# Optimization experiments

Hardware: AMD Instinct MI355X
Metric: run time of the kernel (lower is better)

## Reference

```python
import jax, jax.numpy as jnp
import numpy as np

N_NODES = 100000
N_EDGES = 600000
HIDDEN = 128
BN_EPS = 1e-5


def setup_inputs() -> dict:
    key = jax.random.key(0)
    k_x, k_e, k_w, k_b, k_g = jax.random.split(key, 5)
    x = jax.random.normal(k_x, (N_NODES, HIDDEN), dtype=jnp.float32)
    edge_index = jax.random.randint(k_e, (2, N_EDGES), 0, N_NODES, dtype=jnp.int64)
    # GCNConv linear weight (no bias on the linear; bias added post-aggregation)
    scale = 1.0 / np.sqrt(HIDDEN)
    W = jax.random.uniform(k_w, (HIDDEN, HIDDEN), jnp.float32, -scale, scale)
    b = jax.random.uniform(k_b, (HIDDEN,), jnp.float32, -scale, scale)
    gamma = jnp.ones((HIDDEN,), jnp.float32)   # BatchNorm weight
    beta = jnp.zeros((HIDDEN,), jnp.float32)   # BatchNorm bias
    return {"x": x, "edge_index": edge_index, "W": W, "b": b, "gamma": gamma, "beta": beta}


def reference(x, edge_index, W, b, gamma, beta):
    N = x.shape[0]
    # ReLU then GCNConv linear transform: [N, D]
    h = jnp.matmul(jax.nn.relu(x), W)
    # Add self-loops (PyG GCNConv default)
    loops = jnp.arange(N, dtype=edge_index.dtype)
    row = jnp.concatenate([edge_index[0], loops])  # source nodes
    col = jnp.concatenate([edge_index[1], loops])  # target nodes
    # Symmetric normalization deg^{-1/2} with unit edge weights
    ones = jnp.ones(row.shape[0], dtype=h.dtype)
    deg = jax.ops.segment_sum(ones, col, num_segments=N)
    dinv = jnp.where(deg > 0, jax.lax.rsqrt(deg), 0.0)
    norm = dinv[row] * dinv[col]  # [E+N]
    # Gather -> scale -> scatter-add aggregation, then conv bias
    agg = jax.ops.segment_sum(norm[:, None] * h[row], col, num_segments=N)
    out = agg + b
    # BatchNorm1d (training mode: batch stats, biased variance)
    mean = jnp.mean(out, axis=0)
    var = jnp.var(out, axis=0)
    return gamma * (out - mean) * jax.lax.rsqrt(var + BN_EPS) + beta
```

## Files before the change

### kernel.cpp

```cpp
#include <hip/hip_runtime.h>

#define D 128
#define CAP 32
#define BN_EPS 1e-5f

typedef float floatx4 __attribute__((ext_vector_type(4)));
typedef __bf16 bf16x8 __attribute__((ext_vector_type(8)));

__device__ inline unsigned short f2bf(float f) {
    unsigned u; __builtin_memcpy(&u, &f, 4);
    unsigned r = (u + 0x7FFFu + ((u >> 16) & 1u)) >> 16;
    return (unsigned short)r;
}
__device__ inline float bflo(unsigned v) { unsigned x = v << 16; float f; __builtin_memcpy(&f, &x, 4); return f; }
__device__ inline float bfhi(unsigned v) { unsigned x = v & 0xFFFF0000u; float f; __builtin_memcpy(&f, &x, 4); return f; }

__global__ void setup_k(const unsigned* __restrict__ e, int* __restrict__ flag,
                        int* __restrict__ cursor, float* __restrict__ sums,
                        float* __restrict__ sumsq, const float* __restrict__ W,
                        unsigned short* __restrict__ Wt, int n_nodes) {
    int i = blockIdx.x * blockDim.x + threadIdx.x;
    if (i < n_nodes) cursor[i] = 0;
    if (i < D) { sums[i] = 0.f; sumsq[i] = 0.f; }
    if (i < D * D) {
        int n = i >> 7, k = i & 127;
        Wt[n * D + k] = f2bf(W[k * D + n]);
    }
    if (i == 0) {
        unsigned acc = 0;
        for (int k = 0; k < 64; ++k) acc |= e[2 * k + 1];
        *flag = (acc == 0u) ? 1 : 0;
    }
}

__global__ __launch_bounds__(256, 2) void gemm_k(const float* __restrict__ x,
                                                 const unsigned short* __restrict__ Wt,
                                                 unsigned short* __restrict__ h,
                                                 int n_mtiles) {
    int lane = threadIdx.x & 63;
    int wave = blockIdx.x * 4 + (threadIdx.x >> 6);
    int nw = gridDim.x * 4;
    int l15 = lane & 15;
    int quad = lane >> 4;

    bf16x8 Bf[4][8];
    for (int ks = 0; ks < 4; ++ks)
        for (int j = 0; j < 8; ++j)
            Bf[ks][j] = *(const bf16x8*)(Wt + (size_t)(j * 16 + l15) * D + ks * 32 + quad * 8);

    for (int mt = wave; mt < n_mtiles; mt += nw) {
        const float* xrow = x + (size_t)(mt * 16 + l15) * D + quad * 8;
        bf16x8 Af[4];
        for (int ks = 0; ks < 4; ++ks) {
            float4 a0 = *(const float4*)(xrow + ks * 32);
            float4 a1 = *(const float4*)(xrow + ks * 32 + 4);
            float av[8] = {a0.x, a0.y, a0.z, a0.w, a1.x, a1.y, a1.z, a1.w};
            union { unsigned short u[8]; bf16x8 v; } tmp;
            for (int jj = 0; jj < 8; ++jj) tmp.u[jj] = f2bf(fmaxf(av[jj], 0.0f));
            Af[ks] = tmp.v;
        }
        floatx4 acc[8];
        for (int j = 0; j < 8; ++j) acc[j] = (floatx4){0.f, 0.f, 0.f, 0.f};
        for (int ks = 0; ks < 4; ++ks)
            for (int j = 0; j < 8; ++j)
                acc[j] = __builtin_amdgcn_mfma_f32_16x16x32_bf16(Af[ks], Bf[ks][j], acc[j], 0, 0, 0);
        for (int j = 0; j < 8; ++j)
            for (int reg = 0; reg < 4; ++reg) {
                int rr = mt * 16 + quad * 4 + reg;
                int cc = j * 16 + l15;
                h[(size_t)rr * D + cc] = f2bf(acc[j][reg]);
            }
    }
}

__global__ __launch_bounds__(256) void bucket_k(const void* __restrict__ ep, const int* __restrict__ flag,
                                                int* __restrict__ cursor, int* __restrict__ bucket,
                                                int n_edges) {
    int e = blockIdx.x * blockDim.x + threadIdx.x;
    if (e >= n_edges) return;
    int r, c;
    if (*flag) {
        const long long* p = (const long long*)ep;
        r = (int)p[e]; c = (int)p[e + n_edges];
    } else {
        const int* p = (const int*)ep;
        r = p[e]; c = p[e + n_edges];
    }
    int pos = atomicAdd(&cursor[c], 1);
    if (pos < CAP) bucket[(size_t)c * CAP + pos] = r;
}

__global__ void dinv_k(const int* __restrict__ cursor, float* __restrict__ dinv, int n_nodes) {
    int i = blockIdx.x * blockDim.x + threadIdx.x;
    if (i < n_nodes) dinv[i] = rsqrtf(1.0f + (float)cursor[i]);
}

#define PREPD(s, rr) { int r_ = ((s) < degc) ? (rr) : node;              \
                       w##s = ((s) < degc) ? dinv[r_] : 0.0f;            \
                       hv##s = hp[(unsigned)r_ * 64u + lane]; }
#define ACC(s) { ax += w##s * bflo(hv##s); ay += w##s * bfhi(hv##s); }

__global__ __launch_bounds__(256) void agg_k(const unsigned short* __restrict__ h,
                                             const int* __restrict__ bucket,
                                             const int* __restrict__ cursor,
                                             const float* __restrict__ dinv,
                                             unsigned* __restrict__ aggb,
                                             int n_nodes) {
    int lane = threadIdx.x & 63;
    int node = blockIdx.x * 4 + (threadIdx.x >> 6);
    if (node >= n_nodes) return;
    const unsigned* hp = (const unsigned*)h;

    int deg = cursor[node];
    int degc = deg < CAP ? deg : CAP;
    float dc = dinv[node];

    unsigned v = hp[(unsigned)node * 64u + lane];
    float ax = dc * bflo(v), ay = dc * bfhi(v);
    const int* bk = bucket + (size_t)node * CAP;

    float w0=0,w1=0,w2=0,w3=0,w4=0,w5=0,w6=0,w7=0;
    unsigned hv0=0,hv1=0,hv2=0,hv3=0,hv4=0,hv5=0,hv6=0,hv7=0;

    if (degc > 0) { int4 b = *(const int4*)(bk);     PREPD(0,b.x) PREPD(1,b.y) PREPD(2,b.z) PREPD(3,b.w) }
    if (degc > 4) { int4 b = *(const int4*)(bk + 4); PREPD(4,b.x) PREPD(5,b.y) PREPD(6,b.z) PREPD(7,b.w) }

    if (degc <= 8) {
        ACC(0) ACC(1) ACC(2) ACC(3) ACC(4) ACC(5) ACC(6) ACC(7)
    } else {
        float w8=0,w9=0,w10=0,w11=0,w12=0,w13=0,w14=0,w15=0;
        unsigned hv8=0,hv9=0,hv10=0,hv11=0,hv12=0,hv13=0,hv14=0,hv15=0;
        { int4 b = *(const int4*)(bk + 8); PREPD(8,b.x) PREPD(9,b.y) PREPD(10,b.z) PREPD(11,b.w) }
        if (degc > 12) { int4 b = *(const int4*)(bk + 12); PREPD(12,b.x) PREPD(13,b.y) PREPD(14,b.z) PREPD(15,b.w) }
        ACC(0)  ACC(1)  ACC(2)  ACC(3)  ACC(4)  ACC(5)  ACC(6)  ACC(7)
        ACC(8)  ACC(9)  ACC(10) ACC(11) ACC(12) ACC(13) ACC(14) ACC(15)
        for (int e = 16; e < degc; ++e) {
            int r = bk[e];
            float dr = dinv[r];
            unsigned hh = hp[(unsigned)r * 64u + lane];
            ax += dr * bflo(hh); ay += dr * bfhi(hh);
        }
    }

    float ox = dc * ax, oy = dc * ay;
    aggb[(unsigned)node * 64u + lane] = ((unsigned)f2bf(oy) << 16) | (unsigned)f2bf(ox);
}

__global__ __launch_bounds__(256) void stats_k(const unsigned* __restrict__ aggb,
                                               float* __restrict__ sums, float* __restrict__ sumsq,
                                               int n_nodes) {
    __shared__ float red[256];
    int lane = threadIdx.x & 63;
    int wib = threadIdx.x >> 6;
    int wave = blockIdx.x * 4 + wib;
    int nw = gridDim.x * 4;
    float s0 = 0.f, s1 = 0.f, q0 = 0.f, q1 = 0.f;
    int n = wave;
    for (; n + 3 * nw < n_nodes; n += 4 * nw) {
        unsigned p0 = aggb[(size_t)n * 64 + lane];
        unsigned p1 = aggb[(size_t)(n + nw) * 64 + lane];
        unsigned p2 = aggb[(size_t)(n + 2 * nw) * 64 + lane];
        unsigned p3 = aggb[(size_t)(n + 3 * nw) * 64 + lane];
        float a0 = bflo(p0), b0 = bfhi(p0), a1 = bflo(p1), b1 = bfhi(p1);
        float a2 = bflo(p2), b2 = bfhi(p2), a3 = bflo(p3), b3 = bfhi(p3);
        s0 += a0 + a1 + a2 + a3;
        s1 += b0 + b1 + b2 + b3;
        q0 += a0 * a0 + a1 * a1 + a2 * a2 + a3 * a3;
        q1 += b0 * b0 + b1 * b1 + b2 * b2 + b3 * b3;
    }
    for (; n < n_nodes; n += nw) {
        unsigned p = aggb[(size_t)n * 64 + lane];
        float vx = bflo(p), vy = bfhi(p);
        s0 += vx; s1 += vy; q0 += vx * vx; q1 += vy * vy;
    }
    red[threadIdx.x] = s0; __syncthreads();
    if (wib == 0) atomicAdd(&sums[2 * lane], red[lane] + red[64 + lane] + red[128 + lane] + red[192 + lane]);
    __syncthreads();
    red[threadIdx.x] = s1; __syncthreads();
    if (wib == 0) atomicAdd(&sums[2 * lane + 1], red[lane] + red[64 + lane] + red[128 + lane] + red[192 + lane]);
    __syncthreads();
    red[threadIdx.x] = q0; __syncthreads();
    if (wib == 0) atomicAdd(&sumsq[2 * lane], red[lane] + red[64 + lane] + red[128 + lane] + red[192 + lane]);
    __syncthreads();
    red[threadIdx.x] = q1; __syncthreads();
    if (wib == 0) atomicAdd(&sumsq[2 * lane + 1], red[lane] + red[64 + lane] + red[128 + lane] + red[192 + lane]);
}

__global__ __launch_bounds__(256) void final_k(const unsigned* __restrict__ aggb,
                                               const float* __restrict__ sums, const float* __restrict__ sumsq,
                                               const float* __restrict__ gamma, const float* __restrict__ beta,
                                               float* __restrict__ out, int total4, float inv_n) {
    int i = blockIdx.x * blockDim.x + threadIdx.x;
    if (i >= total4) return;
    int idx = i * 4;
    int f = idx & (D - 1);
    float4 sm = *(const float4*)(sums + f);
    float4 sq = *(const float4*)(sumsq + f);
    float4 g  = *(const float4*)(gamma + f);
    float4 bt = *(const float4*)(beta + f);
    uint2 p = *(const uint2*)(aggb + i * 2);

    float m0 = sm.x * inv_n, m1 = sm.y * inv_n, m2 = sm.z * inv_n, m3 = sm.w * inv_n;
    float sc0 = g.x * rsqrtf(sq.x * inv_n - m0 * m0 + BN_EPS);
    float sc1 = g.y * rsqrtf(sq.y * inv_n - m1 * m1 + BN_EPS);
    float sc2 = g.z * rsqrtf(sq.z * inv_n - m2 * m2 + BN_EPS);
    float sc3 = g.w * rsqrtf(sq.w * inv_n - m3 * m3 + BN_EPS);
    float4 o;
    o.x = fmaf(bflo(p.x), sc0, bt.x - m0 * sc0);
    o.y = fmaf(bfhi(p.x), sc1, bt.y - m1 * sc1);
    o.z = fmaf(bflo(p.y), sc2, bt.z - m2 * sc2);
    o.w = fmaf(bfhi(p.y), sc3, bt.w - m3 * sc3);
    *(float4*)(out + idx) = o;
}

extern "C" void kernel_launch(void* const* d_in, const int* in_sizes, int n_in,
                              void* d_out, int out_size, void* d_ws, size_t ws_size,
                              hipStream_t stream) {
    const float* x     = (const float*)d_in[0];
    const void*  edges = d_in[1];
    const float* W     = (const float*)d_in[2];
    const float* gamma = (const float*)d_in[4];
    const float* beta  = (const float*)d_in[5];
    float* out = (float*)d_out;

    int N = in_sizes[0] / D;
    int E = in_sizes[1] / 2;

    char* ws = (char*)d_ws;
    size_t off = 0;
    auto alloc = [&](size_t bytes) { void* p = ws + off; off += (bytes + 255) & ~(size_t)255; return p; };
    unsigned short* h  = (unsigned short*)alloc((size_t)N * D * 2);
    unsigned* aggb     = (unsigned*)alloc((size_t)N * D * 2);
    int* bucket        = (int*)alloc((size_t)N * CAP * 4);
    int* cursor        = (int*)alloc((size_t)N * 4);
    float* dinv        = (float*)alloc((size_t)N * 4);
    unsigned short* Wt = (unsigned short*)alloc((size_t)D * D * 2);
    float* sums        = (float*)alloc(512);
    float* sumsq       = (float*)alloc(512);
    int* flag          = (int*)alloc(16);

    int nblk = (N + 255) / 256;
    int n_mtiles = N / 16;

    setup_k<<<nblk, 256, 0, stream>>>((const unsigned*)edges, flag, cursor, sums, sumsq, W, Wt, N);
    gemm_k<<<1563, 256, 0, stream>>>(x, Wt, h, n_mtiles);
    bucket_k<<<(E + 255) / 256, 256, 0, stream>>>(edges, flag, cursor, bucket, E);
    dinv_k<<<nblk, 256, 0, stream>>>(cursor, dinv, N);
    agg_k<<<(N + 3) / 4, 256, 0, stream>>>(h, bucket, cursor, dinv, aggb, N);
    stats_k<<<512, 256, 0, stream>>>(aggb, sums, sumsq, N);
    final_k<<<(N * D / 4 + 255) / 256, 256, 0, stream>>>(aggb, sums, sumsq, gamma, beta, out, N * D / 4, 1.0f / (float)N);
}
```

Before: 253.0 us.

## Process two nodes per wave in aggregation and two edges per bucket thread

The aggregation kernel now handles two destination nodes per wavefront and issues all the neighbour gathers for both nodes before accumulating, which raises memory-level parallelism. The bucket kernel handles two edges per thread and is launched before the GEMM. The stats kernel grid grows from 512 to 2048 blocks. The intent is to hide gather latency and reduce launch and tail overhead. The cost is more register pressure and some wasted gathers on padded slots for low-degree nodes.

```diff
diff --git a/kernel.cpp b/kernel.cpp
--- a/kernel.cpp
+++ b/kernel.cpp
@@ -31,6 +31,29 @@
         for (int k = 0; k < 64; ++k) acc |= e[2 * k + 1];
         *flag = (acc == 0u) ? 1 : 0;
     }
+}
+
+__global__ __launch_bounds__(256) void bucket_k(const void* __restrict__ ep, const int* __restrict__ flag,
+                                                int* __restrict__ cursor, int* __restrict__ bucket,
+                                                int n_edges) {
+    int t = blockIdx.x * 256 + threadIdx.x;
+    int e0 = t * 2, e1 = t * 2 + 1;
+    if (e0 >= n_edges) return;
+    bool two = (e1 < n_edges);
+    int r0, c0, r1 = 0, c1 = 0;
+    if (*flag) {
+        const long long* p = (const long long*)ep;
+        r0 = (int)p[e0]; c0 = (int)p[e0 + n_edges];
+        if (two) { r1 = (int)p[e1]; c1 = (int)p[e1 + n_edges]; }
+    } else {
+        const int* p = (const int*)ep;
+        r0 = p[e0]; c0 = p[e0 + n_edges];
+        if (two) { r1 = p[e1]; c1 = p[e1 + n_edges]; }
+    }
+    int pos0 = atomicAdd(&cursor[c0], 1);
+    int pos1 = two ? atomicAdd(&cursor[c1], 1) : CAP;
+    if (pos0 < CAP) bucket[(size_t)c0 * CAP + pos0] = r0;
+    if (pos1 < CAP) bucket[(size_t)c1 * CAP + pos1] = r1;
 }
 
 __global__ __launch_bounds__(256, 2) void gemm_k(const float* __restrict__ x,
@@ -73,32 +96,10 @@
     }
 }
 
-__global__ __launch_bounds__(256) void bucket_k(const void* __restrict__ ep, const int* __restrict__ flag,
-                                                int* __restrict__ cursor, int* __restrict__ bucket,
-                                                int n_edges) {
-    int e = blockIdx.x * blockDim.x + threadIdx.x;
-    if (e >= n_edges) return;
-    int r, c;
-    if (*flag) {
-        const long long* p = (const long long*)ep;
-        r = (int)p[e]; c = (int)p[e + n_edges];
-    } else {
-        const int* p = (const int*)ep;
-        r = p[e]; c = p[e + n_edges];
-    }
-    int pos = atomicAdd(&cursor[c], 1);
-    if (pos < CAP) bucket[(size_t)c * CAP + pos] = r;
-}
-
 __global__ void dinv_k(const int* __restrict__ cursor, float* __restrict__ dinv, int n_nodes) {
     int i = blockIdx.x * blockDim.x + threadIdx.x;
     if (i < n_nodes) dinv[i] = rsqrtf(1.0f + (float)cursor[i]);
 }
-
-#define PREPD(s, rr) { int r_ = ((s) < degc) ? (rr) : node;              \
-                       w##s = ((s) < degc) ? dinv[r_] : 0.0f;            \
-                       hv##s = hp[(unsigned)r_ * 64u + lane]; }
-#define ACC(s) { ax += w##s * bflo(hv##s); ay += w##s * bfhi(hv##s); }
 
 __global__ __launch_bounds__(256) void agg_k(const unsigned short* __restrict__ h,
                                              const int* __restrict__ bucket,
@@ -107,43 +108,71 @@
                                              unsigned* __restrict__ aggb,
                                              int n_nodes) {
     int lane = threadIdx.x & 63;
-    int node = blockIdx.x * 4 + (threadIdx.x >> 6);
-    if (node >= n_nodes) return;
+    int wave = blockIdx.x * 4 + (threadIdx.x >> 6);
+    int n0 = wave * 2;
+    if (n0 >= n_nodes) return;
+    int n1 = n0 + 1;
+    bool one = (n1 >= n_nodes);
+    if (one) n1 = n0;
     const unsigned* hp = (const unsigned*)h;
 
-    int deg = cursor[node];
-    int degc = deg < CAP ? deg : CAP;
-    float dc = dinv[node];
-
-    unsigned v = hp[(unsigned)node * 64u + lane];
-    float ax = dc * bflo(v), ay = dc * bfhi(v);
-    const int* bk = bucket + (size_t)node * CAP;
-
-    float w0=0,w1=0,w2=0,w3=0,w4=0,w5=0,w6=0,w7=0;
-    unsigned hv0=0,hv1=0,hv2=0,hv3=0,hv4=0,hv5=0,hv6=0,hv7=0;
-
-    if (degc > 0) { int4 b = *(const int4*)(bk);     PREPD(0,b.x) PREPD(1,b.y) PREPD(2,b.z) PREPD(3,b.w) }
-    if (degc > 4) { int4 b = *(const int4*)(bk + 4); PREPD(4,b.x) PREPD(5,b.y) PREPD(6,b.z) PREPD(7,b.w) }
-
-    if (degc <= 8) {
-        ACC(0) ACC(1) ACC(2) ACC(3) ACC(4) ACC(5) ACC(6) ACC(7)
-    } else {
-        float w8=0,w9=0,w10=0,w11=0,w12=0,w13=0,w14=0,w15=0;
-        unsigned hv8=0,hv9=0,hv10=0,hv11=0,hv12=0,hv13=0,hv14=0,hv15=0;
-        { int4 b = *(const int4*)(bk + 8); PREPD(8,b.x) PREPD(9,b.y) PREPD(10,b.z) PREPD(11,b.w) }
-        if (degc > 12) { int4 b = *(const int4*)(bk + 12); PREPD(12,b.x) PREPD(13,b.y) PREPD(14,b.z) PREPD(15,b.w) }
-        ACC(0)  ACC(1)  ACC(2)  ACC(3)  ACC(4)  ACC(5)  ACC(6)  ACC(7)
-        ACC(8)  ACC(9)  ACC(10) ACC(11) ACC(12) ACC(13) ACC(14) ACC(15)
-        for (int e = 16; e < degc; ++e) {
-            int r = bk[e];
-            float dr = dinv[r];
-            unsigned hh = hp[(unsigned)r * 64u + lane];
-            ax += dr * bflo(hh); ay += dr * bfhi(hh);
-        }
-    }
-
-    float ox = dc * ax, oy = dc * ay;
-    aggb[(unsigned)node * 64u + lane] = ((unsigned)f2bf(oy) << 16) | (unsigned)f2bf(ox);
+    int deg0 = cursor[n0], deg1 = cursor[n1];
+    int dgc0 = deg0 < CAP ? deg0 : CAP;
+    int dgc1 = deg1 < CAP ? deg1 : CAP;
+    float dc0 = dinv[n0], dc1 = dinv[n1];
+
+    unsigned v0 = hp[(unsigned)n0 * 64u + lane];
+    unsigned v1 = hp[(unsigned)n1 * 64u + lane];
+    float ax0 = dc0 * bflo(v0), ay0 = dc0 * bfhi(v0);
+    float ax1 = dc1 * bflo(v1), ay1 = dc1 * bfhi(v1);
+
+    const int* bk0 = bucket + (size_t)n0 * CAP;
+    const int* bk1 = bucket + (size_t)n1 * CAP;
+    int4 b0a = *(const int4*)(bk0);
+    int4 b0b = *(const int4*)(bk0 + 4);
+    int4 b1a = *(const int4*)(bk1);
+    int4 b1b = *(const int4*)(bk1 + 4);
+    int rr0[8] = {b0a.x, b0a.y, b0a.z, b0a.w, b0b.x, b0b.y, b0b.z, b0b.w};
+    int rr1[8] = {b1a.x, b1a.y, b1a.z, b1a.w, b1b.x, b1b.y, b1b.z, b1b.w};
+
+    float w0[8], w1[8];
+    unsigned hv0[8], hv1[8];
+#pragma unroll
+    for (int s = 0; s < 8; ++s) {
+        int r = (s < dgc0) ? rr0[s] : n0;
+        w0[s] = (s < dgc0) ? dinv[r] : 0.0f;
+        hv0[s] = hp[(unsigned)r * 64u + lane];
+    }
+#pragma unroll
+    for (int s = 0; s < 8; ++s) {
+        int r = (s < dgc1) ? rr1[s] : n1;
+        w1[s] = (s < dgc1) ? dinv[r] : 0.0f;
+        hv1[s] = hp[(unsigned)r * 64u + lane];
+    }
+#pragma unroll
+    for (int s = 0; s < 8; ++s) { ax0 += w0[s] * bflo(hv0[s]); ay0 += w0[s] * bfhi(hv0[s]); }
+#pragma unroll
+    for (int s = 0; s < 8; ++s) { ax1 += w1[s] * bflo(hv1[s]); ay1 += w1[s] * bfhi(hv1[s]); }
+
+    for (int p = 8; p < dgc0; ++p) {
+        int r = bk0[p];
+        float w = dinv[r];
+        unsigned hh = hp[(unsigned)r * 64u + lane];
+        ax0 += w * bflo(hh); ay0 += w * bfhi(hh);
+    }
+    for (int p = 8; p < dgc1; ++p) {
+        int r = bk1[p];
+        float w = dinv[r];
+        unsigned hh = hp[(unsigned)r * 64u + lane];
+        ax1 += w * bflo(hh); ay1 += w * bfhi(hh);
+    }
+
+    float ox0 = dc0 * ax0, oy0 = dc0 * ay0;
+    aggb[(unsigned)n0 * 64u + lane] = ((unsigned)f2bf(oy0) << 16) | (unsigned)f2bf(ox0);
+    if (!one) {
+        float ox1 = dc1 * ax1, oy1 = dc1 * ay1;
+        aggb[(unsigned)n1 * 64u + lane] = ((unsigned)f2bf(oy1) << 16) | (unsigned)f2bf(ox1);
+    }
 }
 
 __global__ __launch_bounds__(256) void stats_k(const unsigned* __restrict__ aggb,
@@ -243,10 +272,10 @@
     int n_mtiles = N / 16;
 
     setup_k<<<nblk, 256, 0, stream>>>((const unsigned*)edges, flag, cursor, sums, sumsq, W, Wt, N);
+    bucket_k<<<((E + 1) / 2 + 255) / 256, 256, 0, stream>>>(edges, flag, cursor, bucket, E);
     gemm_k<<<1563, 256, 0, stream>>>(x, Wt, h, n_mtiles);
-    bucket_k<<<(E + 255) / 256, 256, 0, stream>>>(edges, flag, cursor, bucket, E);
     dinv_k<<<nblk, 256, 0, stream>>>(cursor, dinv, N);
-    agg_k<<<(N + 3) / 4, 256, 0, stream>>>(h, bucket, cursor, dinv, aggb, N);
-    stats_k<<<512, 256, 0, stream>>>(aggb, sums, sumsq, N);
+    agg_k<<<(N / 2 + 3) / 4, 256, 0, stream>>>(h, bucket, cursor, dinv, aggb, N);
+    stats_k<<<2048, 256, 0, stream>>>(aggb, sums, sumsq, N);
     final_k<<<(N * D / 4 + 255) / 256, 256, 0, stream>>>(aggb, sums, sumsq, gamma, beta, out, N * D / 4, 1.0f / (float)N);
 }
```

Result: slower. 318.5 us (+25.9%).
